# Kernel optimization log

Hardware: AMD Instinct MI355X
Metric: run time of the kernel (lower is better)

Reference implementation:

```python
import jax, jax.numpy as jnp
import numpy as np

TEMP = 0.07
LAMBDA_CON = 1.0
LAMBDA_SHELL = 1.0
NEG_INF = -1e30


def setup_inputs() -> dict:
    key = jax.random.key(0)
    k1, k2, k3, k4, k5 = jax.random.split(key, 5)
    B, D = 8192, 1024
    emb = jax.random.normal(k1, (B, D), jnp.float32)
    emb = emb / jnp.linalg.norm(emb, axis=1, keepdims=True)  # encoder outputs are unit-norm
    center = jax.random.normal(k2, (D,), jnp.float32)
    center = center / jnp.linalg.norm(center)  # buffer is F.normalize'd in estimate_epoch_geometry
    labels = jax.random.randint(k3, (B,), 0, 2)  # 0 = machine, 1 = human
    radius_m = jax.random.uniform(k4, (1,), jnp.float32)
    radius_h = radius_m + jax.random.uniform(k5, (1,), jnp.float32)  # radius_h >= radius_m by construction
    return {"embeddings": emb, "center": center, "radius_m": radius_m,
            "radius_h": radius_h, "labels": labels}


def reference(embeddings, center, radius_m, radius_h, labels):
    rm = radius_m[0]
    rh = radius_h[0]
    B = embeddings.shape[0]

    # ---- shell loss ----
    distances = jnp.linalg.norm(embeddings - center[None, :], axis=1)  # [B]
    mmask = labels == 0
    hmask = labels == 1
    nm = jnp.sum(mmask)
    nh = jnp.sum(hmask)
    loss_m = jnp.sum(jnp.where(mmask, jnp.square(jax.nn.relu(distances - rm)), 0.0)) / jnp.maximum(nm, 1)
    loss_h = jnp.sum(jnp.where(hmask, jnp.square(jax.nn.relu(rh - distances)), 0.0)) / jnp.maximum(nh, 1)
    loss_shell = loss_m + loss_h

    # ---- contrastive loss (batched: one BxB sim matrix instead of per-anchor loop) ----
    S = (embeddings @ embeddings.T) / TEMP          # [B, B] pairwise logits
    Sp = (embeddings @ center) / TEMP               # [B]  logits vs prototype
    eye = jnp.eye(B, dtype=bool)
    S_masked = jnp.where(eye, jnp.asarray(NEG_INF, S.dtype), S)
    # denominator per machine anchor i: logsumexp over {other machines, prototype, humans}
    # (labels are only 0/1, so all j != i contribute) plus the prototype logit
    lse = jnp.logaddexp(jax.nn.logsumexp(S_masked, axis=1), Sp)  # [B]
    # positives for machine anchor i: other machines (nm-1) + prototype -> nm positives
    pos_sum = jnp.sum(jnp.where(mmask[None, :] & ~eye, S, 0.0), axis=1) + Sp  # [B]
    anchor_loss = lse - pos_sum / jnp.maximum(nm, 1)
    con_sum = jnp.sum(jnp.where(mmask, anchor_loss, 0.0))
    # prototype as anchor: positives = machines, negatives = humans
    lse_p = jax.nn.logsumexp(Sp)
    proto_loss = lse_p - jnp.sum(jnp.where(mmask, Sp, 0.0)) / jnp.maximum(nm, 1)
    loss_con = (con_sum + proto_loss) / jnp.maximum(nm + 1, 1)
    # original returns 0 when either class is empty
    both = (nm > 0) & (nh > 0)
    loss_con = jnp.where(both, loss_con, 0.0)

    loss = LAMBDA_SHELL * loss_shell + LAMBDA_CON * loss_con
    return (loss, loss_shell, loss_m, loss_h, loss_con, distances)
```

## Files before the change

### kernel.cpp

```cpp
#include <hip/hip_runtime.h>

#define INV_T 14.285714285714286f
#define C1 0.055803571428571425f

typedef float f32x16 __attribute__((ext_vector_type(16)));
typedef float f32x4 __attribute__((ext_vector_type(4)));
typedef int i32x4v __attribute__((ext_vector_type(4)));
typedef int i32x8 __attribute__((ext_vector_type(8)));

__device__ __forceinline__ unsigned char f2e4m3(float f) {
    unsigned char s = (unsigned char)((__float_as_uint(f) >> 24) & 0x80);
    float a = fabsf(f);
    if (a > 448.f) a = 448.f;
    if (a == 0.f) return s;
    int e = (int)((__float_as_uint(a) >> 23) & 0xFF) - 127;
    if (e < -10) return s;
    if (e < -6) e = -6;
    float scale = __int_as_float((unsigned)(130 - e) << 23);
    int mi = (int)rintf(a * scale);
    if (mi >= 16) { mi >>= 1; ++e; }
    if (mi < 8) return s | (unsigned char)mi;
    return s | (unsigned char)(((e + 7) << 3) | (mi - 8));
}

__device__ __forceinline__ void async16(void* l, const void* g) {
    __builtin_amdgcn_global_load_lds(
        (const __attribute__((address_space(1))) unsigned int*)g,
        (__attribute__((address_space(3))) unsigned int*)l, 16, 0, 0);
}

__global__ void __launch_bounds__(256) k_prep(const float* __restrict__ emb,
                                              const float* __restrict__ center,
                                              unsigned char* __restrict__ embQ,
                                              float* __restrict__ out,
                                              float* __restrict__ Sp, int D, int B) {
    int tid = threadIdx.x;
    int wave = tid >> 6, lane = tid & 63;
    int gw = blockIdx.x * 4 + wave;
    int nw = gridDim.x * 4;
    const float4* c4 = (const float4*)center;
    for (int i = gw; i < B; i += nw) {
        const float4* row = (const float4*)(emb + (size_t)i * D);
        uchar4* qrow = embQ ? (uchar4*)(embQ + (size_t)i * D) : nullptr;
        float d2 = 0.f, sp = 0.f;
#pragma unroll
        for (int j = 0; j < 4; ++j) {
            int idx = lane + j * 64;
            float4 e = row[idx];
            float4 c = c4[idx];
            float dx = e.x - c.x, dy = e.y - c.y, dz = e.z - c.z, dw = e.w - c.w;
            d2 += dx * dx + dy * dy + dz * dz + dw * dw;
            sp += e.x * c.x + e.y * c.y + e.z * c.z + e.w * c.w;
            if (qrow)
                qrow[idx] = make_uchar4(f2e4m3(e.x * 16.f), f2e4m3(e.y * 16.f),
                                        f2e4m3(e.z * 16.f), f2e4m3(e.w * 16.f));
        }
#pragma unroll
        for (int m = 1; m <= 32; m <<= 1) {
            d2 += __shfl_xor(d2, m, 64);
            sp += __shfl_xor(sp, m, 64);
        }
        if (lane == 0) {
            out[5 + i] = sqrtf(d2);
            Sp[i] = sp * INV_T;
        }
    }
}

__global__ void __launch_bounds__(256) k_colsum(const float* __restrict__ emb,
                                                const int* __restrict__ labels,
                                                float* __restrict__ s_m,
                                                int* __restrict__ cnt, int D) {
    int t = threadIdx.x;
    int r0 = blockIdx.x * 32;
    float4 acc = {0.f, 0.f, 0.f, 0.f};
#pragma unroll 4
    for (int r = 0; r < 32; ++r) {
        float sc = (labels[r0 + r] == 0) ? 1.f : 0.f;
        float4 v = ((const float4*)(emb + (size_t)(r0 + r) * D))[t];
        acc.x += v.x * sc; acc.y += v.y * sc; acc.z += v.z * sc; acc.w += v.w * sc;
    }
    atomicAdd(&s_m[t * 4 + 0], acc.x);
    atomicAdd(&s_m[t * 4 + 1], acc.y);
    atomicAdd(&s_m[t * 4 + 2], acc.z);
    atomicAdd(&s_m[t * 4 + 3], acc.w);
    if (t == 0) {
        int c = 0;
        for (int r = 0; r < 32; ++r) c += (labels[r0 + r] == 0) ? 1 : 0;
        atomicAdd(cnt, c);
    }
}

#define MXMFMA(a, b, c) __builtin_amdgcn_mfma_scale_f32_32x32x64_f8f6f4( \
    (a), (b), (c), 0, 0, 0, 0x7F7F7F7F, 0, 0x7F7F7F7F)

__global__ void __launch_bounds__(256, 3)
k_sumexp_mx(const unsigned char* __restrict__ embQ, float* __restrict__ sumexp,
            int D, int nT) {
    int bid = blockIdx.x;
    const int n = nT;
    float nf = (float)n + 0.5f;
    int rb = (int)(nf - sqrtf(fmaxf(nf * nf - 2.0f * (float)bid, 0.f)));
    if (rb < 0) rb = 0;
    if (rb > n - 1) rb = n - 1;
#define TRI_OFF(r) ((r) * n - ((r) * ((r)-1)) / 2)
    while (rb + 1 <= n - 1 && TRI_OFF(rb + 1) <= bid) ++rb;
    while (rb > 0 && TRI_OFF(rb) > bid) --rb;
    int cb = rb + (bid - TRI_OFF(rb));
#undef TRI_OFF
    int rowbase = rb * 128, colbase = cb * 128;

    int tid = threadIdx.x;
    int wave = tid >> 6, lane = tid & 63;
    int wr = wave >> 1, wc = wave & 1;
    int l31 = lane & 31, kk = lane >> 5;

    __shared__ unsigned char sA[3][8192];
    __shared__ unsigned char sB[3][8192];
    __shared__ float rred[2][128];
    __shared__ float cred[2][128];

    f32x16 acc[2][2];
#pragma unroll
    for (int fr = 0; fr < 2; ++fr)
#pragma unroll
        for (int fc = 0; fc < 2; ++fc)
#pragma unroll
            for (int v = 0; v < 16; ++v) acc[fr][fc][v] = 0.f;

    const int kG = D >> 6;

    const unsigned char* gA[2];
    const unsigned char* gB[2];
    unsigned int dstOff[2];
#pragma unroll
    for (int q = 0; q < 2; ++q) {
        int ch = q * 256 + tid;
        int L = ch >> 3;
        int t = ch & 7;
        int u = t ^ (L & 7);
        int row = (L << 1) | (u >> 2);
        int s = u & 3;
        gA[q] = embQ + (size_t)(rowbase + row) * D + s * 16;
        gB[q] = embQ + (size_t)(colbase + row) * D + s * 16;
        dstOff[q] = (unsigned)ch << 4;
    }

    auto stage = [&](int buf, int kt) {
        int ko = kt << 6;
        async16(&sA[buf][dstOff[0]], gA[0] + ko);
        async16(&sA[buf][dstOff[1]], gA[1] + ko);
        async16(&sB[buf][dstOff[0]], gB[0] + ko);
        async16(&sB[buf][dstOff[1]], gB[1] + ko);
    };

    int aOff[2][2], bOff[2][2];
#pragma unroll
    for (int f = 0; f < 2; ++f) {
        int ra = wr * 64 + f * 32 + l31;
        int La = ra >> 1, ha = (ra & 1) << 2, wa = La & 7;
        int rbv = wc * 64 + f * 32 + l31;
        int Lb = rbv >> 1, hb = (rbv & 1) << 2, wb = Lb & 7;
#pragma unroll
        for (int j = 0; j < 2; ++j) {
            aOff[f][j] = (La << 7) + (((ha | (kk * 2 + j)) ^ wa) << 4);
            bOff[f][j] = (Lb << 7) + (((hb | (kk * 2 + j)) ^ wb) << 4);
        }
    }

    stage(0, 0);
    if (kG > 1) stage(1, 1);

    int cur = 0;
    for (int kt = 0; kt < kG; ++kt) {
        if (kt + 1 < kG) {
            asm volatile("s_waitcnt vmcnt(4)" ::: "memory");
        } else {
            asm volatile("s_waitcnt vmcnt(0)" ::: "memory");
        }
        __builtin_amdgcn_s_barrier();
        if (kt + 2 < kG) {
            int nxt = cur + 2;
            if (nxt >= 3) nxt -= 3;
            stage(nxt, kt + 2);
        }
        const unsigned char* A = sA[cur];
        const unsigned char* Bp = sB[cur];
        i32x8 av[2], bv[2];
#pragma unroll
        for (int f = 0; f < 2; ++f) {
            i32x4v lo = *(const i32x4v*)&A[aOff[f][0]];
            i32x4v hi = *(const i32x4v*)&A[aOff[f][1]];
            av[f] = __builtin_shufflevector(lo, hi, 0, 1, 2, 3, 4, 5, 6, 7);
            i32x4v lo2 = *(const i32x4v*)&Bp[bOff[f][0]];
            i32x4v hi2 = *(const i32x4v*)&Bp[bOff[f][1]];
            bv[f] = __builtin_shufflevector(lo2, hi2, 0, 1, 2, 3, 4, 5, 6, 7);
        }
        __builtin_amdgcn_s_setprio(1);
#pragma unroll
        for (int fr = 0; fr < 2; ++fr)
#pragma unroll
            for (int fc = 0; fc < 2; ++fc)
                acc[fr][fc] = MXMFMA(av[fr], bv[fc], acc[fr][fc]);
        __builtin_amdgcn_s_setprio(0);
        if (++cur == 3) cur = 0;
    }

    float rs[2][16];
    float cs[2] = {0.f, 0.f};
#pragma unroll
    for (int fr = 0; fr < 2; ++fr)
#pragma unroll
        for (int v = 0; v < 16; ++v) rs[fr][v] = 0.f;

#pragma unroll
    for (int fr = 0; fr < 2; ++fr)
#pragma unroll
        for (int fc = 0; fc < 2; ++fc) {
            int gcol = colbase + wc * 64 + fc * 32 + l31;
#pragma unroll
            for (int v = 0; v < 16; ++v) {
                int grow = rowbase + wr * 64 + fr * 32 + (v & 3) + 8 * (v >> 2) + 4 * kk;
                float e = (grow < gcol) ? __expf(acc[fr][fc][v] * C1 - INV_T) : 0.f;
                rs[fr][v] += e;
                cs[fc] += e;
            }
        }

#pragma unroll
    for (int m = 1; m <= 16; m <<= 1)
#pragma unroll
        for (int fr = 0; fr < 2; ++fr)
#pragma unroll
            for (int v = 0; v < 16; ++v) rs[fr][v] += __shfl_xor(rs[fr][v], m, 64);
    if (l31 == 0)
#pragma unroll
        for (int fr = 0; fr < 2; ++fr)
#pragma unroll
            for (int v = 0; v < 16; ++v)
                rred[wc][wr * 64 + fr * 32 + (v & 3) + 8 * (v >> 2) + 4 * kk] = rs[fr][v];

#pragma unroll
    for (int fc = 0; fc < 2; ++fc) cs[fc] += __shfl_xor(cs[fc], 32, 64);
    if (kk == 0)
#pragma unroll
        for (int fc = 0; fc < 2; ++fc) cred[wr][wc * 64 + fc * 32 + l31] = cs[fc];

    __syncthreads();
    if (tid < 128) {
        atomicAdd(&sumexp[rowbase + tid], rred[0][tid] + rred[1][tid]);
    } else {
        int u = tid - 128;
        atomicAdd(&sumexp[colbase + u], cred[0][u] + cred[1][u]);
    }
}

typedef __bf16 bf16x8 __attribute__((ext_vector_type(8)));
typedef unsigned short u16x8 __attribute__((ext_vector_type(8)));
__device__ __forceinline__ unsigned short f2bf(float f) {
    unsigned int x = __float_as_uint(f);
    x += 0x7fffu + ((x >> 16) & 1u);
    return (unsigned short)(x >> 16);
}
__global__ void __launch_bounds__(256) k_sumexp_fb(const float* __restrict__ embF,
                                                   float* __restrict__ sumexp, int D, int nTiles) {
    int bid = blockIdx.x;
    const int n = nTiles;
    float nf = (float)n + 0.5f;
    int rb = (int)(nf - sqrtf(fmaxf(nf * nf - 2.0f * (float)bid, 0.f)));
    if (rb < 0) rb = 0;
    if (rb > n - 1) rb = n - 1;
#define TRI_OFF(r) ((r) * n - ((r) * ((r)-1)) / 2)
    while (rb + 1 <= n - 1 && TRI_OFF(rb + 1) <= bid) ++rb;
    while (rb > 0 && TRI_OFF(rb) > bid) --rb;
    int cb = rb + (bid - TRI_OFF(rb));
#undef TRI_OFF
    int tid = threadIdx.x;
    int wave = tid >> 6, lane = tid & 63;
    int wr = wave >> 1, wc = wave & 1;
    int quad = lane >> 4, l15 = lane & 15;
    int rowbase = rb * 128, colbase = cb * 128;
    __shared__ unsigned short lA[128 * 64];
    __shared__ unsigned short lB[128 * 64];
    __shared__ float rred[2][128];
    __shared__ float cred[2][128];
    f32x4 zero = {0.f, 0.f, 0.f, 0.f};
    f32x4 acc[4][4];
#pragma unroll
    for (int r = 0; r < 4; ++r)
#pragma unroll
        for (int c = 0; c < 4; ++c) acc[r][c] = zero;
    const int kIters = D >> 6;
    for (int kt = 0; kt < kIters; ++kt) {
        int k0 = kt << 6;
#pragma unroll
        for (int q = 0; q < 4; ++q) {
            int ch = q * 256 + tid;
            int row = ch >> 3, lc = ch & 7;
            int pc = lc ^ (row & 7);
            const float4* sa = (const float4*)(embF + (size_t)(rowbase + row) * D + k0 + lc * 8);
            const float4* sb = (const float4*)(embF + (size_t)(colbase + row) * D + k0 + lc * 8);
            float4 a0 = sa[0], a1 = sa[1];
            float4 b0 = sb[0], b1 = sb[1];
            u16x8 va = {f2bf(a0.x), f2bf(a0.y), f2bf(a0.z), f2bf(a0.w),
                        f2bf(a1.x), f2bf(a1.y), f2bf(a1.z), f2bf(a1.w)};
            u16x8 vb = {f2bf(b0.x), f2bf(b0.y), f2bf(b0.z), f2bf(b0.w),
                        f2bf(b1.x), f2bf(b1.y), f2bf(b1.z), f2bf(b1.w)};
            *(u16x8*)&lA[(row << 6) + (pc << 3)] = va;
            *(u16x8*)&lB[(row << 6) + (pc << 3)] = vb;
        }
        __syncthreads();
#pragma unroll
        for (int h = 0; h < 2; ++h) {
            bf16x8 af[4], bfr[4];
#pragma unroll
            for (int r = 0; r < 4; ++r) {
                int row = wr * 64 + r * 16 + l15;
                int pc = (h * 4 + quad) ^ (l15 & 7);
                af[r] = *(const bf16x8*)&lA[(row << 6) + (pc << 3)];
            }
#pragma unroll
            for (int c = 0; c < 4; ++c) {
                int row = wc * 64 + c * 16 + l15;
                int pc = (h * 4 + quad) ^ (l15 & 7);
                bfr[c] = *(const bf16x8*)&lB[(row << 6) + (pc << 3)];
            }
#pragma unroll
            for (int r = 0; r < 4; ++r)
#pragma unroll
                for (int c = 0; c < 4; ++c)
                    acc[r][c] = __builtin_amdgcn_mfma_f32_16x16x32_bf16(af[r], bfr[c], acc[r][c], 0, 0, 0);
        }
        __syncthreads();
    }
    float rs[4][4], cs[4];
#pragma unroll
    for (int r = 0; r < 4; ++r)
#pragma unroll
        for (int v = 0; v < 4; ++v) rs[r][v] = 0.f;
#pragma unroll
    for (int c = 0; c < 4; ++c) cs[c] = 0.f;
#pragma unroll
    for (int r = 0; r < 4; ++r)
#pragma unroll
        for (int c = 0; c < 4; ++c) {
            f32x4 a = acc[r][c];
            int gcol = colbase + wc * 64 + c * 16 + l15;
#pragma unroll
            for (int v = 0; v < 4; ++v) {
                int grow = rowbase + wr * 64 + r * 16 + quad * 4 + v;
                float e = (grow < gcol) ? __expf((a[v] - 1.0f) * INV_T) : 0.f;
                rs[r][v] += e;
                cs[c] += e;
            }
        }
#pragma unroll
    for (int m = 1; m <= 8; m <<= 1)
#pragma unroll
        for (int r = 0; r < 4; ++r)
#pragma unroll
            for (int v = 0; v < 4; ++v) rs[r][v] += __shfl_xor(rs[r][v], m, 64);
    if (l15 == 0)
#pragma unroll
        for (int r = 0; r < 4; ++r)
#pragma unroll
            for (int v = 0; v < 4; ++v)
                rred[wc][wr * 64 + r * 16 + quad * 4 + v] = rs[r][v];
#pragma unroll
    for (int m = 16; m <= 32; m <<= 1)
#pragma unroll
        for (int c = 0; c < 4; ++c) cs[c] += __shfl_xor(cs[c], m, 64);
    if (quad == 0)
#pragma unroll
        for (int c = 0; c < 4; ++c) cred[wr][wc * 64 + c * 16 + l15] = cs[c];
    __syncthreads();
    if (tid < 128) {
        atomicAdd(&sumexp[rowbase + tid], rred[0][tid] + rred[1][tid]);
    } else {
        int u = tid & 127;
        atomicAdd(&sumexp[colbase + u], cred[0][u] + cred[1][u]);
    }
}

__global__ void __launch_bounds__(256) k_finalize(const float* __restrict__ emb,
                                                  const float* __restrict__ s_m,
                                                  const float* __restrict__ Sp,
                                                  const float* __restrict__ sumexp,
                                                  const int* __restrict__ labels,
                                                  const float* __restrict__ outv,
                                                  const float* __restrict__ rmp,
                                                  const float* __restrict__ rhp,
                                                  float* __restrict__ scal, int D) {
    int tid = threadIdx.x;
    int wave = tid >> 6, lane = tid & 63;
    __shared__ float ac[8];
    if (tid < 8) ac[tid] = 0.f;
    __syncthreads();
    float rm = rmp[0], rh = rhp[0];
    const float4* sm4 = (const float4*)s_m;
    for (int it = 0; it < 8; ++it) {
        int i = blockIdx.x * 32 + it * 4 + wave;
        const float4* row = (const float4*)(emb + (size_t)i * D);
        float q = 0.f, sd = 0.f;
#pragma unroll
        for (int j = 0; j < 4; ++j) {
            int idx = lane + j * 64;
            float4 e = row[idx];
            float4 s = sm4[idx];
            q += e.x * s.x + e.y * s.y + e.z * s.z + e.w * s.w;
            sd += e.x * e.x + e.y * e.y + e.z * e.z + e.w * e.w;
        }
#pragma unroll
        for (int m = 1; m <= 32; m <<= 1) {
            q += __shfl_xor(q, m, 64);
            sd += __shfl_xor(sd, m, 64);
        }
        if (lane == 0) {
            float LP = Sp[i];
            float eS = __expf(LP - INV_T);
            float lse = INV_T + __logf(sumexp[i] + eS);
            bool mach = (labels[i] == 0);
            float pos = (q - (mach ? sd : 0.f)) * INV_T + LP;
            float d = outv[5 + i];
            atomicAdd(&ac[2], eS);
            if (mach) {
                atomicAdd(&ac[4], lse);
                atomicAdd(&ac[5], pos);
                atomicAdd(&ac[3], LP);
                float x = d - rm;
                if (x > 0.f) atomicAdd(&ac[0], x * x);
            } else {
                float x = rh - d;
                if (x > 0.f) atomicAdd(&ac[1], x * x);
            }
        }
    }
    __syncthreads();
    if (tid < 8) atomicAdd(&scal[tid], ac[tid]);
}

__global__ void k_final(const float* __restrict__ scal, const int* __restrict__ cnt,
                        float* __restrict__ out, int B) {
    if (threadIdx.x == 0) {
        int nm = cnt[0], nh = B - nm;
        float nmf = (float)(nm > 1 ? nm : 1);
        float nhf = (float)(nh > 1 ? nh : 1);
        float loss_m = scal[0] / nmf;
        float loss_h = scal[1] / nhf;
        float loss_shell = loss_m + loss_h;
        float lse_p = INV_T + __logf(scal[2]);
        float proto = lse_p - scal[3] / nmf;
        float con = scal[4] - scal[5] / nmf;
        int denom = (nm + 1 > 1) ? nm + 1 : 1;
        float lc = (con + proto) / (float)denom;
        if (!(nm > 0 && nh > 0)) lc = 0.f;
        out[0] = loss_shell + lc;
        out[1] = loss_shell;
        out[2] = loss_m;
        out[3] = loss_h;
        out[4] = lc;
    }
}

extern "C" void kernel_launch(void* const* d_in, const int* in_sizes, int n_in,
                              void* d_out, int out_size, void* d_ws, size_t ws_size,
                              hipStream_t stream) {
    const float* emb = (const float*)d_in[0];
    const float* center = (const float*)d_in[1];
    const float* rmp = (const float*)d_in[2];
    const float* rhp = (const float*)d_in[3];
    const int* labels = (const int*)d_in[4];
    float* out = (float*)d_out;
    const int B = in_sizes[4];
    const int D = in_sizes[1];

    size_t qBytes = (size_t)B * D;
    size_t auxBytes = (size_t)B * 4 + (size_t)D * 4 + 256 + (size_t)B * 4;
    bool pre = ws_size >= qBytes + auxBytes;
    size_t Z0 = pre ? qBytes : 0;

    char* ws = (char*)d_ws;
    unsigned char* embQ = (unsigned char*)ws;
    float* sumexp = (float*)(ws + Z0);
    float* s_m = (float*)(ws + Z0 + (size_t)B * 4);
    float* scal = (float*)(ws + Z0 + (size_t)B * 4 + (size_t)D * 4);
    int* cnt = (int*)(scal + 8);
    float* Sp = (float*)(ws + Z0 + (size_t)B * 4 + (size_t)D * 4 + 256);

    hipMemsetAsync(ws + Z0, 0, (size_t)B * 4 + (size_t)D * 4 + 256, stream);

    k_prep<<<512, 256, 0, stream>>>(emb, center, pre ? embQ : nullptr, out, Sp, D, B);
    k_colsum<<<B / 32, D / 4, 0, stream>>>(emb, labels, s_m, cnt, D);

    int nT = B / 128;
    int nBlocks = nT * (nT + 1) / 2;
    if (pre) k_sumexp_mx<<<nBlocks, 256, 0, stream>>>(embQ, sumexp, D, nT);
    else     k_sumexp_fb<<<nBlocks, 256, 0, stream>>>(emb, sumexp, D, nT);

    k_finalize<<<B / 32, 256, 0, stream>>>(emb, s_m, Sp, sumexp, labels, out, rmp, rhp, scal, D);
    k_final<<<1, 64, 0, stream>>>(scal, cnt, out, B);
}
```

Measured before the change: 195.8 us.

## Enlarge FP8 MFMA sim tiles to 256x256 with 512-thread blocks and XCD remap

The upper-triangular similarity kernel now uses 256x256 output tiles computed by 8 waves (each 128x64), instead of 128x128 tiles with 4 waves. This raises arithmetic intensity per byte staged into LDS and cuts the number of workgroups and global atomics. The LDS layout and swizzle are rewritten for the new tile shape. A block-index remap spreads consecutive tiles across the 8 XCDs, and a sched_barrier is added after the barrier. The trade-offs are doubled LDS use and more accumulator registers per wave, which may reduce occupancy, plus fewer blocks to balance across CUs.

```diff
diff --git a/kernel.cpp b/kernel.cpp
--- a/kernel.cpp
+++ b/kernel.cpp
@@ -27,6 +27,12 @@
     __builtin_amdgcn_global_load_lds(
         (const __attribute__((address_space(1))) unsigned int*)g,
         (__attribute__((address_space(3))) unsigned int*)l, 16, 0, 0);
+}
+
+__device__ __forceinline__ i32x8 rd8(const unsigned char* p0, const unsigned char* p1) {
+    i32x4v lo = *(const i32x4v*)p0;
+    i32x4v hi = *(const i32x4v*)p1;
+    return __builtin_shufflevector(lo, hi, 0, 1, 2, 3, 4, 5, 6, 7);
 }
 
 __global__ void __launch_bounds__(256) k_prep(const float* __restrict__ emb,
@@ -94,11 +100,16 @@
 #define MXMFMA(a, b, c) __builtin_amdgcn_mfma_scale_f32_32x32x64_f8f6f4( \
     (a), (b), (c), 0, 0, 0, 0x7F7F7F7F, 0, 0x7F7F7F7F)
 
-__global__ void __launch_bounds__(256, 3)
+__global__ void __launch_bounds__(512, 2)
 k_sumexp_mx(const unsigned char* __restrict__ embQ, float* __restrict__ sumexp,
             int D, int nT) {
+    const int n = nT;
+    int nwg = n * (n + 1) / 2;
     int bid = blockIdx.x;
-    const int n = nT;
+    if ((nwg & 7) == 0) {
+        int cpx = nwg >> 3;
+        bid = (bid & 7) * cpx + (bid >> 3);
+    }
     float nf = (float)n + 0.5f;
     int rb = (int)(nf - sqrtf(fmaxf(nf * nf - 2.0f * (float)bid, 0.f)));
     if (rb < 0) rb = 0;
@@ -108,21 +119,21 @@
     while (rb > 0 && TRI_OFF(rb) > bid) --rb;
     int cb = rb + (bid - TRI_OFF(rb));
 #undef TRI_OFF
-    int rowbase = rb * 128, colbase = cb * 128;
+    int rowbase = rb * 256, colbase = cb * 256;
 
     int tid = threadIdx.x;
     int wave = tid >> 6, lane = tid & 63;
-    int wr = wave >> 1, wc = wave & 1;
+    int wr = wave >> 2, wc = wave & 3;
     int l31 = lane & 31, kk = lane >> 5;
 
-    __shared__ unsigned char sA[3][8192];
-    __shared__ unsigned char sB[3][8192];
-    __shared__ float rred[2][128];
-    __shared__ float cred[2][128];
-
-    f32x16 acc[2][2];
-#pragma unroll
-    for (int fr = 0; fr < 2; ++fr)
+    __shared__ unsigned char sA[3][16384];
+    __shared__ unsigned char sB[3][16384];
+    __shared__ float rred[4][256];
+    __shared__ float cred[2][256];
+
+    f32x16 acc[4][2];
+#pragma unroll
+    for (int fr = 0; fr < 4; ++fr)
 #pragma unroll
         for (int fc = 0; fc < 2; ++fc)
 #pragma unroll
@@ -130,42 +141,43 @@
 
     const int kG = D >> 6;
 
-    const unsigned char* gA[2];
-    const unsigned char* gB[2];
+    const unsigned char* gSA[2];
+    const unsigned char* gSB[2];
     unsigned int dstOff[2];
 #pragma unroll
     for (int q = 0; q < 2; ++q) {
-        int ch = q * 256 + tid;
-        int L = ch >> 3;
-        int t = ch & 7;
-        int u = t ^ (L & 7);
-        int row = (L << 1) | (u >> 2);
-        int s = u & 3;
-        gA[q] = embQ + (size_t)(rowbase + row) * D + s * 16;
-        gB[q] = embQ + (size_t)(colbase + row) * D + s * 16;
+        int ch = q * 512 + tid;
+        int r = ch >> 2;
+        int s = (ch & 3) ^ ((r >> 1) & 3);
+        gSA[q] = embQ + (size_t)(rowbase + r) * D + s * 16;
+        gSB[q] = embQ + (size_t)(colbase + r) * D + s * 16;
         dstOff[q] = (unsigned)ch << 4;
     }
 
     auto stage = [&](int buf, int kt) {
         int ko = kt << 6;
-        async16(&sA[buf][dstOff[0]], gA[0] + ko);
-        async16(&sA[buf][dstOff[1]], gA[1] + ko);
-        async16(&sB[buf][dstOff[0]], gB[0] + ko);
-        async16(&sB[buf][dstOff[1]], gB[1] + ko);
+        async16(&sA[buf][dstOff[0]], gSA[0] + ko);
+        async16(&sA[buf][dstOff[1]], gSA[1] + ko);
+        async16(&sB[buf][dstOff[0]], gSB[0] + ko);
+        async16(&sB[buf][dstOff[1]], gSB[1] + ko);
     };
 
-    int aOff[2][2], bOff[2][2];
-#pragma unroll
-    for (int f = 0; f < 2; ++f) {
-        int ra = wr * 64 + f * 32 + l31;
-        int La = ra >> 1, ha = (ra & 1) << 2, wa = La & 7;
-        int rbv = wc * 64 + f * 32 + l31;
-        int Lb = rbv >> 1, hb = (rbv & 1) << 2, wb = Lb & 7;
-#pragma unroll
-        for (int j = 0; j < 2; ++j) {
-            aOff[f][j] = (La << 7) + (((ha | (kk * 2 + j)) ^ wa) << 4);
-            bOff[f][j] = (Lb << 7) + (((hb | (kk * 2 + j)) ^ wb) << 4);
-        }
+    int aOff[4][2], bOff[2][2];
+#pragma unroll
+    for (int fr = 0; fr < 4; ++fr) {
+        int r = wr * 128 + fr * 32 + l31;
+        int w = (r >> 1) & 3;
+#pragma unroll
+        for (int j = 0; j < 2; ++j)
+            aOff[fr][j] = r * 64 + (((kk * 2 + j) ^ w) << 4);
+    }
+#pragma unroll
+    for (int fc = 0; fc < 2; ++fc) {
+        int r = wc * 64 + fc * 32 + l31;
+        int w = (r >> 1) & 3;
+#pragma unroll
+        for (int j = 0; j < 2; ++j)
+            bOff[fc][j] = r * 64 + (((kk * 2 + j) ^ w) << 4);
     }
 
     stage(0, 0);
@@ -179,6 +191,7 @@
             asm volatile("s_waitcnt vmcnt(0)" ::: "memory");
         }
         __builtin_amdgcn_s_barrier();
+        __builtin_amdgcn_sched_barrier(0);
         if (kt + 2 < kG) {
             int nxt = cur + 2;
             if (nxt >= 3) nxt -= 3;
@@ -186,19 +199,16 @@
         }
         const unsigned char* A = sA[cur];
         const unsigned char* Bp = sB[cur];
-        i32x8 av[2], bv[2];
-#pragma unroll
-        for (int f = 0; f < 2; ++f) {
-            i32x4v lo = *(const i32x4v*)&A[aOff[f][0]];
-            i32x4v hi = *(const i32x4v*)&A[aOff[f][1]];
-            av[f] = __builtin_shufflevector(lo, hi, 0, 1, 2, 3, 4, 5, 6, 7);
-            i32x4v lo2 = *(const i32x4v*)&Bp[bOff[f][0]];
-            i32x4v hi2 = *(const i32x4v*)&Bp[bOff[f][1]];
-            bv[f] = __builtin_shufflevector(lo2, hi2, 0, 1, 2, 3, 4, 5, 6, 7);
-        }
+        i32x8 av[4], bv[2];
+#pragma unroll
+        for (int fr = 0; fr < 4; ++fr)
+            av[fr] = rd8(A + aOff[fr][0], A + aOff[fr][1]);
+#pragma unroll
+        for (int fc = 0; fc < 2; ++fc)
+            bv[fc] = rd8(Bp + bOff[fc][0], Bp + bOff[fc][1]);
         __builtin_amdgcn_s_setprio(1);
 #pragma unroll
-        for (int fr = 0; fr < 2; ++fr)
+        for (int fr = 0; fr < 4; ++fr)
 #pragma unroll
             for (int fc = 0; fc < 2; ++fc)
                 acc[fr][fc] = MXMFMA(av[fr], bv[fc], acc[fr][fc]);
@@ -206,51 +216,45 @@
         if (++cur == 3) cur = 0;
     }
 
-    float rs[2][16];
     float cs[2] = {0.f, 0.f};
 #pragma unroll
-    for (int fr = 0; fr < 2; ++fr)
-#pragma unroll
-        for (int v = 0; v < 16; ++v) rs[fr][v] = 0.f;
-
-#pragma unroll
-    for (int fr = 0; fr < 2; ++fr)
+    for (int fr = 0; fr < 4; ++fr) {
+        float rs[16];
+#pragma unroll
+        for (int v = 0; v < 16; ++v) rs[v] = 0.f;
 #pragma unroll
         for (int fc = 0; fc < 2; ++fc) {
             int gcol = colbase + wc * 64 + fc * 32 + l31;
 #pragma unroll
             for (int v = 0; v < 16; ++v) {
-                int grow = rowbase + wr * 64 + fr * 32 + (v & 3) + 8 * (v >> 2) + 4 * kk;
+                int grow = rowbase + wr * 128 + fr * 32 + (v & 3) + 8 * (v >> 2) + 4 * kk;
                 float e = (grow < gcol) ? __expf(acc[fr][fc][v] * C1 - INV_T) : 0.f;
-                rs[fr][v] += e;
+                rs[v] += e;
                 cs[fc] += e;
             }
         }
-
-#pragma unroll
-    for (int m = 1; m <= 16; m <<= 1)
-#pragma unroll
-        for (int fr = 0; fr < 2; ++fr)
-#pragma unroll
-            for (int v = 0; v < 16; ++v) rs[fr][v] += __shfl_xor(rs[fr][v], m, 64);
-    if (l31 == 0)
-#pragma unroll
-        for (int fr = 0; fr < 2; ++fr)
+#pragma unroll
+        for (int m = 1; m <= 16; m <<= 1)
+#pragma unroll
+            for (int v = 0; v < 16; ++v) rs[v] += __shfl_xor(rs[v], m, 64);
+        if (l31 == 0)
 #pragma unroll
             for (int v = 0; v < 16; ++v)
-                rred[wc][wr * 64 + fr * 32 + (v & 3) + 8 * (v >> 2) + 4 * kk] = rs[fr][v];
-
-#pragma unroll
-    for (int fc = 0; fc < 2; ++fc) cs[fc] += __shfl_xor(cs[fc], 32, 64);
-    if (kk == 0)
-#pragma unroll
-        for (int fc = 0; fc < 2; ++fc) cred[wr][wc * 64 + fc * 32 + l31] = cs[fc];
+                rred[wc][wr * 128 + fr * 32 + (v & 3) + 8 * (v >> 2) + 4 * kk] = rs[v];
+    }
+    cs[0] += __shfl_xor(cs[0], 32, 64);
+    cs[1] += __shfl_xor(cs[1], 32, 64);
+    if (kk == 0) {
+        cred[wr][wc * 64 + l31] = cs[0];
+        cred[wr][wc * 64 + 32 + l31] = cs[1];
+    }
 
     __syncthreads();
-    if (tid < 128) {
-        atomicAdd(&sumexp[rowbase + tid], rred[0][tid] + rred[1][tid]);
+    if (tid < 256) {
+        atomicAdd(&sumexp[rowbase + tid],
+                  rred[0][tid] + rred[1][tid] + rred[2][tid] + rred[3][tid]);
     } else {
-        int u = tid - 128;
+        int u = tid - 256;
         atomicAdd(&sumexp[colbase + u], cred[0][u] + cred[1][u]);
     }
 }
@@ -476,7 +480,7 @@
 
     size_t qBytes = (size_t)B * D;
     size_t auxBytes = (size_t)B * 4 + (size_t)D * 4 + 256 + (size_t)B * 4;
-    bool pre = ws_size >= qBytes + auxBytes;
+    bool pre = (ws_size >= qBytes + auxBytes) && (B % 256 == 0) && (D % 64 == 0);
     size_t Z0 = pre ? qBytes : 0;
 
     char* ws = (char*)d_ws;
@@ -492,10 +496,15 @@
     k_prep<<<512, 256, 0, stream>>>(emb, center, pre ? embQ : nullptr, out, Sp, D, B);
     k_colsum<<<B / 32, D / 4, 0, stream>>>(emb, labels, s_m, cnt, D);
 
-    int nT = B / 128;
-    int nBlocks = nT * (nT + 1) / 2;
-    if (pre) k_sumexp_mx<<<nBlocks, 256, 0, stream>>>(embQ, sumexp, D, nT);
-    else     k_sumexp_fb<<<nBlocks, 256, 0, stream>>>(emb, sumexp, D, nT);
+    if (pre) {
+        int nT = B / 256;
+        int nBlocks = nT * (nT + 1) / 2;
+        k_sumexp_mx<<<nBlocks, 512, 0, stream>>>(embQ, sumexp, D, nT);
+    } else {
+        int nT = B / 128;
+        int nBlocks = nT * (nT + 1) / 2;
+        k_sumexp_fb<<<nBlocks, 256, 0, stream>>>(emb, sumexp, D, nT);
+    }
 
     k_finalize<<<B / 32, 256, 0, stream>>>(emb, s_m, Sp, sumexp, labels, out, rmp, rhp, scal, D);
     k_final<<<1, 64, 0, stream>>>(scal, cnt, out, B);
```

Measured after the change: 220.1 us. 1.12x slower.
